# Optimization experiments

Hardware: AMD Instinct MI355X
Metric: run time of the kernel (lower is better)

The kernel has to match this reference:

```python
import jax, jax.numpy as jnp
import numpy as np

B, N, DIM, H, DH = 2, 2048, 1024, 16, 64
ALPHA = 32.0 ** 2  # stable_softmax alpha
SCALE = DH ** -0.5


def rotate_half(x):
    # interleaved pairs: (x0, x1, x2, x3, ...) -> (-x1, x0, -x3, x2, ...)
    xp = x.reshape(x.shape[:-1] + (-1, 2))
    return jnp.stack((-xp[..., 1], xp[..., 0]), axis=-1).reshape(x.shape)


def apply_rotary(freqs, t):
    # freqs: [n, d]; t: [b, h, n, d]
    return t * jnp.cos(freqs) + rotate_half(t) * jnp.sin(freqs)


def setup_inputs() -> dict:
    key = jax.random.key(0)
    k0, k1, k2, k3 = jax.random.split(key, 4)
    x = jax.random.normal(k0, (B, N, DIM), jnp.float32)
    rotary_pos_emb = jax.random.normal(k1, (N, DH), jnp.float32)
    w_qkv = jax.random.normal(k2, (DIM, 3 * H * DH), jnp.float32) / np.sqrt(DIM)
    w_out = jax.random.normal(k3, (H * DH, DIM), jnp.float32) / np.sqrt(H * DH)
    b_out = jnp.zeros((DIM,), jnp.float32)
    return {"x": x, "rotary_pos_emb": rotary_pos_emb, "w_qkv": w_qkv,
            "w_out": w_out, "b_out": b_out}


def reference(x, rotary_pos_emb, w_qkv, w_out, b_out):
    b, n, _ = x.shape
    qkv = x @ w_qkv                                  # [b, n, 3*h*d]
    q, k, v = jnp.split(qkv, 3, axis=-1)
    to_heads = lambda t: t.reshape(b, n, H, DH).transpose(0, 2, 1, 3)  # [b,h,n,d]
    q, k, v = map(to_heads, (q, k, v))
    freqs = rotary_pos_emb[:n]
    # source applies rotary emb to q, k AND v
    q = apply_rotary(freqs, q)
    k = apply_rotary(freqs, k)
    v = apply_rotary(freqs, v)
    q = q * SCALE
    dots = jnp.einsum('bhid,bhjd->bhij', q, k)       # [b,h,n,n]
    mask_value = -jnp.finfo(dots.dtype).max
    causal = jnp.triu(jnp.ones((n, n), bool), 1)
    dots = jnp.where(causal, mask_value, dots)
    # stable softmax: divide by alpha, subtract detached max, rescale
    t = dots / ALPHA
    t = t - jax.lax.stop_gradient(jnp.max(t, axis=-1, keepdims=True))
    attn = jax.nn.softmax(t * ALPHA, axis=-1)
    out = jnp.einsum('bhij,bhjd->bhid', attn, v)     # [b,h,n,d]
    out = out.transpose(0, 2, 1, 3).reshape(b, n, H * DH)
    return out @ w_out + b_out
```

## Files before the change

kernel.cpp:

```cpp
#include <hip/hip_runtime.h>
#include <stdint.h>

#define DEV __device__ __forceinline__

typedef __bf16 bf16x8 __attribute__((ext_vector_type(8)));
typedef float  f32x4  __attribute__((ext_vector_type(4)));
typedef short  s16x8  __attribute__((ext_vector_type(8)));

constexpr int Bb   = 2;
constexpr int Nn   = 2048;
constexpr int DIMc = 1024;
constexpr int Hh   = 16;
constexpr int DHc  = 64;
constexpr int BN   = Bb * Nn;
constexpr int QKVC = 3 * Hh * DHc;

DEV ushort f2b(float f) {
  uint32_t u = __float_as_uint(f);
  u += 0x7fffu + ((u >> 16) & 1u);
  return (ushort)(u >> 16);
}

DEV void gload16(const void* g, void* l) {
  __builtin_amdgcn_global_load_lds(
      (const __attribute__((address_space(1))) void*)(uintptr_t)g,
      (__attribute__((address_space(3))) void*)(uint32_t)(uintptr_t)l,
      16, 0, 0);
}

DEV f32x4 mfma16(bf16x8 a, bf16x8 b, f32x4 c) {
  return __builtin_amdgcn_mfma_f32_16x16x32_bf16(a, b, c, 0, 0, 0);
}

DEV uint32_t cvtpk(float lo, float hi) {
  uint32_t r;
  asm("v_cvt_pk_bf16_f32 %0, %1, %2" : "=v"(r) : "v"(lo), "v"(hi));
  return r;
}


__global__ void k_cast_x(const float* __restrict__ x, ushort* __restrict__ xb) {
  int i = blockIdx.x * 256 + threadIdx.x;
  size_t base = (size_t)i * 8;
  s16x8 v;
#pragma unroll
  for (int j = 0; j < 8; ++j) v[j] = (short)f2b(x[base + j]);
  *(s16x8*)(xb + base) = v;
}

__global__ void k_sincos(const float* __restrict__ rope, float2* __restrict__ csT) {
  int i = blockIdx.x * 256 + threadIdx.x;
  float t = rope[i];
  float s, c;
  sincosf(t, &s, &c);
  csT[i] = make_float2(c, s);
}

__global__ void k_transpose_cast(const float* __restrict__ src, ushort* __restrict__ dst,
                                 int K, int Ncols) {
  __shared__ float tile[32][33];
  int nb = blockIdx.x * 32, kb = blockIdx.y * 32;
  int tx = threadIdx.x, ty = threadIdx.y;
#pragma unroll
  for (int i = 0; i < 4; ++i) {
    int k = ty + i * 8;
    tile[k][tx] = src[(size_t)(kb + k) * Ncols + nb + tx];
  }
  __syncthreads();
#pragma unroll
  for (int i = 0; i < 4; ++i) {
    int n = ty + i * 8;
    dst[(size_t)(nb + n) * K + kb + tx] = f2b(tile[tx][n]);
  }
}

DEV void gemm_core(const ushort* __restrict__ A, const ushort* __restrict__ Bt,
                   int rowBase, int colBase, ushort* lA, ushort* lB,
                   f32x4 (&acc)[4][4]) {
  const int tid = threadIdx.x;
  const int lane = tid & 63, w = tid >> 6;
  const int wm = w >> 1, wn = w & 1;
  const int g = lane >> 4, l16 = lane & 15;
  const f32x4 zero = {0.f, 0.f, 0.f, 0.f};
#pragma unroll
  for (int i = 0; i < 4; ++i)
#pragma unroll
    for (int j = 0; j < 4; ++j) acc[i][j] = zero;

  const int c0row = tid >> 2,          c0kc = (tid & 3) ^ ((c0row >> 1) & 3);
  const int c1row = (256 + tid) >> 2,  c1kc = (tid & 3) ^ ((c1row >> 1) & 3);
  const ushort* gA0 = A  + (size_t)(rowBase + c0row) * DIMc + c0kc * 8;
  const ushort* gA1 = A  + (size_t)(rowBase + c1row) * DIMc + c1kc * 8;
  const ushort* gB0 = Bt + (size_t)(colBase + c0row) * DIMc + c0kc * 8;
  const ushort* gB1 = Bt + (size_t)(colBase + c1row) * DIMc + c1kc * 8;
  ushort* lDst0 = (ushort*)((size_t)(0 * 256 + w * 64) * 8 * 2);
  const size_t o0 = (size_t)(0 * 256 + w * 64) * 8;
  const size_t o1 = (size_t)(1 * 256 + w * 64) * 8;

  gload16(gA0, lA + o0);
  gload16(gB0, lB + o0);
  gload16(gA1, lA + o1);
  gload16(gB1, lB + o1);

  for (int k0 = 0; k0 < DIMc; k0 += 32) {
    const int cur = (k0 >> 5) & 1;
    ushort* cA = lA + cur * (128 * 32);
    ushort* cB = lB + cur * (128 * 32);
    if (k0 + 32 < DIMc) {
      ushort* nA = lA + (cur ^ 1) * (128 * 32);
      ushort* nB = lB + (cur ^ 1) * (128 * 32);
      int kn = k0 + 32;
      gload16(gA0 + kn, nA + o0);
      gload16(gB0 + kn, nB + o0);
      gload16(gA1 + kn, nA + o1);
      gload16(gB1 + kn, nB + o1);
      asm volatile("s_waitcnt vmcnt(4)" ::: "memory");
    } else {
      asm volatile("s_waitcnt vmcnt(0)" ::: "memory");
    }
    __builtin_amdgcn_s_barrier();

    bf16x8 af[4], bfr[4];
#pragma unroll
    for (int f = 0; f < 4; ++f) {
      int r  = wm * 64 + f * 16 + l16;
      int r2 = wn * 64 + f * 16 + l16;
      af[f]  = *(const bf16x8*)&cA[r * 32 + ((g ^ ((r >> 1) & 3)) << 3)];
      bfr[f] = *(const bf16x8*)&cB[r2 * 32 + ((g ^ ((r2 >> 1) & 3)) << 3)];
    }
#pragma unroll
    for (int i = 0; i < 4; ++i)
#pragma unroll
      for (int j = 0; j < 4; ++j)
        acc[i][j] = mfma16(af[i], bfr[j], acc[i][j]);

    __builtin_amdgcn_s_barrier();
  }
}

__global__ __launch_bounds__(256) void k_gemm_qkv(
    const ushort* __restrict__ xb, const ushort* __restrict__ wT,
    const float2* __restrict__ csT,
    ushort* __restrict__ Qd, ushort* __restrict__ Kd, ushort* __restrict__ Vd) {
  __shared__ ushort lA[2 * 128 * 32];
  __shared__ ushort lB[2 * 128 * 32];
  f32x4 acc[4][4];
  const int rowBase = blockIdx.y * 128, colBase = blockIdx.x * 128;
  gemm_core(xb, wT, rowBase, colBase, lA, lB, acc);

  const int lane = threadIdx.x & 63, w = threadIdx.x >> 6;
  const int wm = w >> 1, wn = w & 1;
  const int g = lane >> 4, l16 = lane & 15;
#pragma unroll
  for (int fm = 0; fm < 4; ++fm) {
#pragma unroll
    for (int fn = 0; fn < 4; ++fn) {
      int col = colBase + wn * 64 + fn * 16 + l16;
      int sel = col >> 10, hc = col & 1023;
      int h = hc >> 6, d = hc & 63;
      float sgn = (d & 1) ? 1.f : -1.f;
#pragma unroll
      for (int r = 0; r < 4; ++r) {
        float t  = acc[fm][fn][r];
        float tp = __shfl_xor(t, 1);
        int row = rowBase + wm * 64 + fm * 16 + 4 * g + r;
        int b = row >> 11, n = row & 2047;
        float2 cs = csT[n * 64 + d];
        float rv = t * cs.x + sgn * tp * cs.y;
        if (sel == 0) {
          Qd[((size_t)(b * Hh + h) * Nn + n) * DHc + d] = f2b(rv * 0.125f);
        } else if (sel == 1) {
          Kd[((size_t)(b * Hh + h) * Nn + n) * DHc + d] = f2b(rv);
        } else {
          Vd[((size_t)(b * Hh + h) * DHc + d) * Nn + n] = f2b(rv);
        }
      }
    }
  }
}


DEV void stageKV(const ushort* __restrict__ Kh, const ushort* __restrict__ Vh,
                 ushort* lKb, ushort* lVb, int kt, int tid, int w) {
#pragma unroll
  for (int s = 0; s < 2; ++s) {
    int c = s * 256 + tid;
    int row = c >> 3, jst = c & 7;
    int jl = jst ^ (row & 7);
    gload16(Kh + (size_t)(kt * 64 + row) * DHc + jl * 8,
            lKb + (size_t)(s * 256 + w * 64) * 8);
    gload16(Vh + (size_t)row * Nn + kt * 64 + jl * 8,
            lVb + (size_t)(s * 256 + w * 64) * 8);
  }
}

DEV void attn_step(const ushort* lKc, const ushort* lVc, char* lPw,
                   const bf16x8 (&q)[2], f32x4 (&o)[4], float& m, float& l,
                   int kBase, int qg, bool diag, int g, int l16) {
  const f32x4 zero = {0.f, 0.f, 0.f, 0.f};
  f32x4 s[4];
#pragma unroll
  for (int jt = 0; jt < 4; ++jt) s[jt] = zero;

#pragma unroll
  for (int jt = 0; jt < 4; ++jt) {
    int jr = jt * 16 + l16;
#pragma unroll
    for (int d0 = 0; d0 < 2; ++d0) {
      bf16x8 kb = *(const bf16x8*)&lKc[jr * 64 + (((d0 * 4 + g) ^ (jr & 7)) << 3)];
      s[jt] = mfma16(kb, q[d0], s[jt]);
    }
  }

  if (diag) {
#pragma unroll
    for (int jt = 0; jt < 4; ++jt)
#pragma unroll
      for (int r = 0; r < 4; ++r) {
        int j = kBase + jt * 16 + 4 * g + r;
        if (j > qg) s[jt][r] = -3.0e38f;
      }
  }

  float tmax = fmaxf(fmaxf(fmaxf(s[0][0], s[0][1]), fmaxf(s[0][2], s[0][3])),
                     fmaxf(fmaxf(s[1][0], s[1][1]), fmaxf(s[1][2], s[1][3])));
  tmax = fmaxf(tmax, fmaxf(fmaxf(fmaxf(s[2][0], s[2][1]), fmaxf(s[2][2], s[2][3])),
                           fmaxf(fmaxf(s[3][0], s[3][1]), fmaxf(s[3][2], s[3][3]))));
  tmax = fmaxf(tmax, __shfl_xor(tmax, 16));
  tmax = fmaxf(tmax, __shfl_xor(tmax, 32));

  if (!__all(tmax <= m + 8.f)) {
    float mnew = fmaxf(m, tmax);
    float sc = __expf(m - mnew);
#pragma unroll
    for (int dt = 0; dt < 4; ++dt) o[dt] *= sc;
    l *= sc;
    m = mnew;
  }

  float ps = 0.f;
#pragma unroll
  for (int jt = 0; jt < 4; ++jt)
#pragma unroll
    for (int r = 0; r < 4; ++r) {
      float p = __expf(s[jt][r] - m);
      s[jt][r] = p;
      ps += p;
    }
  ps += __shfl_xor(ps, 16);
  ps += __shfl_xor(ps, 32);
  l += ps;

  const int sw = (l16 & 7) << 4;
  char* prow = lPw + l16 * 128;
#pragma unroll
  for (int jt = 0; jt < 4; ++jt) {
    int jo = (jt * 16 + 4 * g) * 2;
    *(uint32_t*)(prow + (jo ^ sw))       = cvtpk(s[jt][0], s[jt][1]);
    *(uint32_t*)(prow + ((jo + 4) ^ sw)) = cvtpk(s[jt][2], s[jt][3]);
  }

  bf16x8 pa[2];
#pragma unroll
  for (int jh = 0; jh < 2; ++jh)
    pa[jh] = *(const bf16x8*)(prow + (((jh * 32 + 8 * g) * 2) ^ sw));
#pragma unroll
  for (int dt = 0; dt < 4; ++dt) {
    int d = dt * 16 + l16;
#pragma unroll
    for (int jh = 0; jh < 2; ++jh) {
      bf16x8 vb = *(const bf16x8*)&lVc[d * 64 + (((jh * 4 + g) ^ (d & 7)) << 3)];
      o[dt] = mfma16(vb, pa[jh], o[dt]);
    }
  }
}

DEV void attn_epi(ushort* __restrict__ ao, int bh, int n, int g,
                  f32x4 (&o)[4], float l) {
  const int b = bh >> 4, h = bh & 15;
  float inv = 1.f / l;
  ushort* dst = ao + (size_t)(b * Nn + n) * (Hh * DHc) + h * 64;
#pragma unroll
  for (int dt = 0; dt < 4; ++dt) {
    uint2 pkd;
    pkd.x = cvtpk(o[dt][0] * inv, o[dt][1] * inv);
    pkd.y = cvtpk(o[dt][2] * inv, o[dt][3] * inv);
    *(uint2*)(dst + dt * 16 + 4 * g) = pkd;
  }
}

__global__ __launch_bounds__(256) void k_attn(
    const ushort* __restrict__ Qd, const ushort* __restrict__ Kd,
    const ushort* __restrict__ Vd, ushort* __restrict__ ao) {
  __shared__ ushort lK[2][64 * 64];
  __shared__ ushort lV[2][64 * 64];
  __shared__ char   lP[4][16 * 128];
  const int tid = threadIdx.x;
  const int lane = tid & 63, w = tid >> 6;
  const int g = lane >> 4, l16 = lane & 15;
  const int bh = blockIdx.y;
  const int p = blockIdx.x;
  const int tA = p, tB = 31 - p;
  const int last = tB;
  const ushort* Qh = Qd + (size_t)bh * Nn * DHc;
  const ushort* Kh = Kd + (size_t)bh * Nn * DHc;
  const ushort* Vh = Vd + (size_t)bh * DHc * Nn;

  const int qgA = tA * 64 + w * 16 + l16;
  const int qgB = tB * 64 + w * 16 + l16;

  bf16x8 qA[2], qB[2];
#pragma unroll
  for (int d0 = 0; d0 < 2; ++d0) {
    qA[d0] = *(const bf16x8*)(Qh + (size_t)qgA * DHc + d0 * 32 + g * 8);
    qB[d0] = *(const bf16x8*)(Qh + (size_t)qgB * DHc + d0 * 32 + g * 8);
  }

  const f32x4 zero = {0.f, 0.f, 0.f, 0.f};
  f32x4 oA[4], oB[4];
#pragma unroll
  for (int dt = 0; dt < 4; ++dt) { oA[dt] = zero; oB[dt] = zero; }
  float mA = -3.0e38f, lA_ = 0.f, mB = -3.0e38f, lB_ = 0.f;

  stageKV(Kh, Vh, lK[0], lV[0], 0, tid, w);

  for (int kt = 0; kt <= last; ++kt) {
    const int cur = kt & 1;
    if (kt < last) {
      stageKV(Kh, Vh, lK[cur ^ 1], lV[cur ^ 1], kt + 1, tid, w);
      asm volatile("s_waitcnt vmcnt(4)" ::: "memory");
    } else {
      asm volatile("s_waitcnt vmcnt(0)" ::: "memory");
    }
    __builtin_amdgcn_s_barrier();

    attn_step(lK[cur], lV[cur], lP[w], qB, oB, mB, lB_, kt * 64, qgB, kt == tB, g, l16);
    if (kt <= tA)
      attn_step(lK[cur], lV[cur], lP[w], qA, oA, mA, lA_, kt * 64, qgA, kt == tA, g, l16);

    __builtin_amdgcn_s_barrier();
  }

  attn_epi(ao, bh, qgA, g, oA, lA_);
  attn_epi(ao, bh, qgB, g, oB, lB_);
}

__global__ __launch_bounds__(256) void k_gemm_out(
    const ushort* __restrict__ ao, const ushort* __restrict__ wT,
    const float* __restrict__ bias, float* __restrict__ out) {
  __shared__ ushort lA[2 * 128 * 32];
  __shared__ ushort lB[2 * 128 * 32];
  f32x4 acc[4][4];
  const int rowBase = blockIdx.y * 128, colBase = blockIdx.x * 128;
  gemm_core(ao, wT, rowBase, colBase, lA, lB, acc);

  const int lane = threadIdx.x & 63, w = threadIdx.x >> 6;
  const int wm = w >> 1, wn = w & 1;
  const int g = lane >> 4, l16 = lane & 15;
#pragma unroll
  for (int fm = 0; fm < 4; ++fm)
#pragma unroll
    for (int fn = 0; fn < 4; ++fn) {
      int col = colBase + wn * 64 + fn * 16 + l16;
#pragma unroll
      for (int r = 0; r < 4; ++r) {
        int row = rowBase + wm * 64 + fm * 16 + 4 * g + r;
        out[(size_t)row * DIMc + col] = acc[fm][fn][r] + bias[col];
      }
    }
}

extern "C" void kernel_launch(void* const* d_in, const int* in_sizes, int n_in,
                              void* d_out, int out_size, void* d_ws, size_t ws_size,
                              hipStream_t stream) {
  const float* x     = (const float*)d_in[0];
  const float* rope  = (const float*)d_in[1];
  const float* w_qkv = (const float*)d_in[2];
  const float* w_out = (const float*)d_in[3];
  const float* b_out = (const float*)d_in[4];
  float* out = (float*)d_out;

  char* ws = (char*)d_ws;
  ushort* xb    = (ushort*)(ws);
  ushort* wqkvT = (ushort*)(ws + 8388608);
  ushort* woutT = (ushort*)(ws + 14680064);
  float2* csT   = (float2*)(ws + 16777216);
  ushort* Qd    = (ushort*)(ws + 17825792);
  ushort* Kd    = (ushort*)(ws + 26214400);
  ushort* Vd    = (ushort*)(ws + 34603008);
  ushort* ao    = (ushort*)(ws + 42991616);

  hipLaunchKernelGGL(k_cast_x, dim3(2048), dim3(256), 0, stream, x, xb);
  hipLaunchKernelGGL(k_transpose_cast, dim3(QKVC / 32, DIMc / 32), dim3(32, 8), 0, stream,
                     w_qkv, wqkvT, DIMc, QKVC);
  hipLaunchKernelGGL(k_transpose_cast, dim3(DIMc / 32, DIMc / 32), dim3(32, 8), 0, stream,
                     w_out, woutT, DIMc, DIMc);
  hipLaunchKernelGGL(k_sincos, dim3(Nn * DHc / 256), dim3(256), 0, stream, rope, csT);
  hipLaunchKernelGGL(k_gemm_qkv, dim3(QKVC / 128, BN / 128), dim3(256), 0, stream,
                     xb, wqkvT, csT, Qd, Kd, Vd);
  hipLaunchKernelGGL(k_attn, dim3(16, Bb * Hh), dim3(256), 0, stream, Qd, Kd, Vd, ao);
  hipLaunchKernelGGL(k_gemm_out, dim3(DIMc / 128, BN / 128), dim3(256), 0, stream,
                     ao, woutT, b_out, out);
}
```

Before: 135.6 us.

## Rewrite QKV GEMM with 256x256 tiles, 8 waves, and interleaved load/MFMA schedule

Replaces the QKV projection GEMM, which used 128x128 tiles and 4 waves, with a 256x256-tile kernel of 8 waves that stages 64-wide K slices. Global-to-LDS loads for the next tile are interleaved between four MFMA quadrants, with explicit barriers, waitcnt and setprio to overlap memory with compute. This aims to raise data reuse and hide load latency. The grid shrinks to 12x16=192 blocks, which may underfill the 256 CUs and raises register pressure.

After: 150.3 us. 1.11x slower.

```diff
diff --git a/kernel.cpp b/kernel.cpp
--- a/kernel.cpp
+++ b/kernel.cpp
@@ -71,6 +71,169 @@
   for (int i = 0; i < 4; ++i) {
     int n = ty + i * 8;
     dst[(size_t)(nb + n) * K + kb + tx] = f2b(tile[tx][n]);
+  }
+}
+
+__global__ __launch_bounds__(512, 2) void k_gemm_qkv(
+    const ushort* __restrict__ xb, const ushort* __restrict__ wT,
+    const float2* __restrict__ csT,
+    ushort* __restrict__ Qd, ushort* __restrict__ Kd, ushort* __restrict__ Vd) {
+  __shared__ ushort lA[2 * 256 * 64];
+  __shared__ ushort lB[2 * 256 * 64];
+  const int tid = threadIdx.x;
+  const int lane = tid & 63, wid = tid >> 6;
+  const int wm = wid >> 2, wn = wid & 3;
+  const int g = lane >> 4, l16 = lane & 15, l7 = lane & 7;
+  const int rowBase = blockIdx.y * 256, colBase = blockIdx.x * 256;
+  constexpr int NT = DIMc / 64;
+
+  const int sr0 = tid >> 3;
+  const int gc  = (tid & 7) ^ (sr0 & 7);
+  const ushort* gA = xb + (size_t)(rowBase + sr0) * DIMc + gc * 8;
+  const ushort* gB = wT + (size_t)(colBase + sr0) * DIMc + gc * 8;
+
+#define STAGE_A(T, H) do { \
+    gload16(gA + (size_t)((H) * 128) * DIMc + (T) * 64, lA + (((T) & 1) * 16384 + (H) * 8192 + wid * 512)); \
+    gload16(gA + (size_t)((H) * 128 + 64) * DIMc + (T) * 64, lA + (((T) & 1) * 16384 + (H) * 8192 + 4096 + wid * 512)); \
+  } while (0)
+#define STAGE_B(T, H) do { \
+    gload16(gB + (size_t)((H) * 128) * DIMc + (T) * 64, lB + (((T) & 1) * 16384 + (H) * 8192 + wid * 512)); \
+    gload16(gB + (size_t)((H) * 128 + 64) * DIMc + (T) * 64, lB + (((T) & 1) * 16384 + (H) * 8192 + 4096 + wid * 512)); \
+  } while (0)
+
+  f32x4 acc[8][4];
+  const f32x4 zero = {0.f, 0.f, 0.f, 0.f};
+#pragma unroll
+  for (int i = 0; i < 8; ++i)
+#pragma unroll
+    for (int j = 0; j < 4; ++j) acc[i][j] = zero;
+
+  bf16x8 aF[4][2], bF[4][2];
+
+  STAGE_A(0, 0); STAGE_A(0, 1); STAGE_B(0, 0); STAGE_B(0, 1);
+  STAGE_B(1, 0); STAGE_B(1, 1);
+  asm volatile("s_waitcnt vmcnt(4)" ::: "memory");
+  __builtin_amdgcn_s_barrier();
+
+  for (int kt = 0; kt < NT; ++kt) {
+    const ushort* cA = lA + (kt & 1) * 16384;
+    const ushort* cB = lB + (kt & 1) * 16384;
+
+#pragma unroll
+    for (int mf = 0; mf < 4; ++mf)
+#pragma unroll
+      for (int ks = 0; ks < 2; ++ks)
+        aF[mf][ks] = *(const bf16x8*)&cA[(wm * 128 + mf * 16 + l16) * 64 + (((ks * 4 + g) ^ l7) << 3)];
+#pragma unroll
+    for (int nf = 0; nf < 2; ++nf)
+#pragma unroll
+      for (int ks = 0; ks < 2; ++ks)
+        bF[nf][ks] = *(const bf16x8*)&cB[(wn * 64 + nf * 16 + l16) * 64 + (((ks * 4 + g) ^ l7) << 3)];
+    if (kt + 1 < NT) STAGE_A(kt + 1, 0);
+    __builtin_amdgcn_s_barrier();
+    asm volatile("s_waitcnt lgkmcnt(0)" ::: "memory");
+    __builtin_amdgcn_sched_barrier(0);
+    __builtin_amdgcn_s_setprio(1);
+#pragma unroll
+    for (int mf = 0; mf < 4; ++mf)
+#pragma unroll
+      for (int nf = 0; nf < 2; ++nf)
+#pragma unroll
+        for (int ks = 0; ks < 2; ++ks)
+          acc[mf][nf] = mfma16(aF[mf][ks], bF[nf][ks], acc[mf][nf]);
+    __builtin_amdgcn_s_setprio(0);
+    __builtin_amdgcn_sched_barrier(0);
+    __builtin_amdgcn_s_barrier();
+
+#pragma unroll
+    for (int nf = 0; nf < 2; ++nf)
+#pragma unroll
+      for (int ks = 0; ks < 2; ++ks)
+        bF[2 + nf][ks] = *(const bf16x8*)&cB[(wn * 64 + (2 + nf) * 16 + l16) * 64 + (((ks * 4 + g) ^ l7) << 3)];
+    if (kt + 1 < NT) STAGE_A(kt + 1, 1);
+    __builtin_amdgcn_s_barrier();
+    asm volatile("s_waitcnt lgkmcnt(0)" ::: "memory");
+    __builtin_amdgcn_sched_barrier(0);
+    __builtin_amdgcn_s_setprio(1);
+#pragma unroll
+    for (int mf = 0; mf < 4; ++mf)
+#pragma unroll
+      for (int nf = 0; nf < 2; ++nf)
+#pragma unroll
+        for (int ks = 0; ks < 2; ++ks)
+          acc[mf][2 + nf] = mfma16(aF[mf][ks], bF[2 + nf][ks], acc[mf][2 + nf]);
+    __builtin_amdgcn_s_setprio(0);
+    __builtin_amdgcn_sched_barrier(0);
+    __builtin_amdgcn_s_barrier();
+
+#pragma unroll
+    for (int mf = 0; mf < 4; ++mf)
+#pragma unroll
+      for (int ks = 0; ks < 2; ++ks)
+        aF[mf][ks] = *(const bf16x8*)&cA[(wm * 128 + 64 + mf * 16 + l16) * 64 + (((ks * 4 + g) ^ l7) << 3)];
+    if (kt + 2 < NT) STAGE_B(kt + 2, 0);
+    __builtin_amdgcn_s_barrier();
+    asm volatile("s_waitcnt lgkmcnt(0)" ::: "memory");
+    __builtin_amdgcn_sched_barrier(0);
+    __builtin_amdgcn_s_setprio(1);
+#pragma unroll
+    for (int mf = 0; mf < 4; ++mf)
+#pragma unroll
+      for (int nf = 0; nf < 2; ++nf)
+#pragma unroll
+        for (int ks = 0; ks < 2; ++ks)
+          acc[4 + mf][nf] = mfma16(aF[mf][ks], bF[nf][ks], acc[4 + mf][nf]);
+    __builtin_amdgcn_s_setprio(0);
+    __builtin_amdgcn_sched_barrier(0);
+    __builtin_amdgcn_s_barrier();
+
+    if (kt + 2 < NT) {
+      STAGE_B(kt + 2, 1);
+      asm volatile("s_waitcnt vmcnt(4)" ::: "memory");
+    } else {
+      asm volatile("s_waitcnt vmcnt(0)" ::: "memory");
+    }
+    __builtin_amdgcn_s_barrier();
+    __builtin_amdgcn_s_setprio(1);
+#pragma unroll
+    for (int mf = 0; mf < 4; ++mf)
+#pragma unroll
+      for (int nf = 0; nf < 2; ++nf)
+#pragma unroll
+        for (int ks = 0; ks < 2; ++ks)
+          acc[4 + mf][2 + nf] = mfma16(aF[mf][ks], bF[2 + nf][ks], acc[4 + mf][2 + nf]);
+    __builtin_amdgcn_s_setprio(0);
+    __builtin_amdgcn_sched_barrier(0);
+    __builtin_amdgcn_s_barrier();
+  }
+#undef STAGE_A
+#undef STAGE_B
+
+#pragma unroll
+  for (int mf = 0; mf < 8; ++mf) {
+#pragma unroll
+    for (int nf = 0; nf < 4; ++nf) {
+      int col = colBase + wn * 64 + nf * 16 + l16;
+      int sel = col >> 10, hc = col & 1023;
+      int h = hc >> 6, d = hc & 63;
+      float sgn = (d & 1) ? 1.f : -1.f;
+#pragma unroll
+      for (int r = 0; r < 4; ++r) {
+        float t  = acc[mf][nf][r];
+        float tp = __shfl_xor(t, 1);
+        int row = rowBase + wm * 128 + mf * 16 + 4 * g + r;
+        int b = row >> 11, n = row & 2047;
+        float2 cs = csT[n * 64 + d];
+        float rv = t * cs.x + sgn * tp * cs.y;
+        if (sel == 0) {
+          Qd[((size_t)(b * Hh + h) * Nn + n) * DHc + d] = f2b(rv * 0.125f);
+        } else if (sel == 1) {
+          Kd[((size_t)(b * Hh + h) * Nn + n) * DHc + d] = f2b(rv);
+        } else {
+          Vd[((size_t)(b * Hh + h) * DHc + d) * Nn + n] = f2b(rv);
+        }
+      }
+    }
   }
 }
 
@@ -93,7 +256,6 @@
   const ushort* gA1 = A  + (size_t)(rowBase + c1row) * DIMc + c1kc * 8;
   const ushort* gB0 = Bt + (size_t)(colBase + c0row) * DIMc + c0kc * 8;
   const ushort* gB1 = Bt + (size_t)(colBase + c1row) * DIMc + c1kc * 8;
-  ushort* lDst0 = (ushort*)((size_t)(0 * 256 + w * 64) * 8 * 2);
   const size_t o0 = (size_t)(0 * 256 + w * 64) * 8;
   const size_t o1 = (size_t)(1 * 256 + w * 64) * 8;
 
@@ -135,47 +297,6 @@
         acc[i][j] = mfma16(af[i], bfr[j], acc[i][j]);
 
     __builtin_amdgcn_s_barrier();
-  }
-}
-
-__global__ __launch_bounds__(256) void k_gemm_qkv(
-    const ushort* __restrict__ xb, const ushort* __restrict__ wT,
-    const float2* __restrict__ csT,
-    ushort* __restrict__ Qd, ushort* __restrict__ Kd, ushort* __restrict__ Vd) {
-  __shared__ ushort lA[2 * 128 * 32];
-  __shared__ ushort lB[2 * 128 * 32];
-  f32x4 acc[4][4];
-  const int rowBase = blockIdx.y * 128, colBase = blockIdx.x * 128;
-  gemm_core(xb, wT, rowBase, colBase, lA, lB, acc);
-
-  const int lane = threadIdx.x & 63, w = threadIdx.x >> 6;
-  const int wm = w >> 1, wn = w & 1;
-  const int g = lane >> 4, l16 = lane & 15;
-#pragma unroll
-  for (int fm = 0; fm < 4; ++fm) {
-#pragma unroll
-    for (int fn = 0; fn < 4; ++fn) {
-      int col = colBase + wn * 64 + fn * 16 + l16;
-      int sel = col >> 10, hc = col & 1023;
-      int h = hc >> 6, d = hc & 63;
-      float sgn = (d & 1) ? 1.f : -1.f;
-#pragma unroll
-      for (int r = 0; r < 4; ++r) {
-        float t  = acc[fm][fn][r];
-        float tp = __shfl_xor(t, 1);
-        int row = rowBase + wm * 64 + fm * 16 + 4 * g + r;
-        int b = row >> 11, n = row & 2047;
-        float2 cs = csT[n * 64 + d];
-        float rv = t * cs.x + sgn * tp * cs.y;
-        if (sel == 0) {
-          Qd[((size_t)(b * Hh + h) * Nn + n) * DHc + d] = f2b(rv * 0.125f);
-        } else if (sel == 1) {
-          Kd[((size_t)(b * Hh + h) * Nn + n) * DHc + d] = f2b(rv);
-        } else {
-          Vd[((size_t)(b * Hh + h) * DHc + d) * Nn + n] = f2b(rv);
-        }
-      }
-    }
   }
 }
 
@@ -396,7 +517,7 @@
   hipLaunchKernelGGL(k_transpose_cast, dim3(DIMc / 32, DIMc / 32), dim3(32, 8), 0, stream,
                      w_out, woutT, DIMc, DIMc);
   hipLaunchKernelGGL(k_sincos, dim3(Nn * DHc / 256), dim3(256), 0, stream, rope, csT);
-  hipLaunchKernelGGL(k_gemm_qkv, dim3(QKVC / 128, BN / 128), dim3(256), 0, stream,
+  hipLaunchKernelGGL(k_gemm_qkv, dim3(QKVC / 256, BN / 256), dim3(512), 0, stream,
                      xb, wqkvT, csT, Qd, Kd, Vd);
   hipLaunchKernelGGL(k_attn, dim3(16, Bb * Hh), dim3(256), 0, stream, Qd, Kd, Vd, ao);
   hipLaunchKernelGGL(k_gemm_out, dim3(DIMc / 128, BN / 128), dim3(256), 0, stream,
```

## Triple-buffer GEMM LDS tiles with one barrier per k-step

Applied to the files above, without the earlier changes.

Changes the shared GEMM core from a double-buffered to a three-stage LDS pipeline. Loads are issued two k-steps ahead, and each iteration now has a single barrier instead of two. The aim is to hide global-to-LDS latency behind the MFMA work and cut synchronisation in the QKV and output projection GEMMs. The cost is 50% more LDS per block, which may lower occupancy.

New measurement: 131.1 us. 1.03x faster.

```diff
diff --git a/kernel.cpp b/kernel.cpp
--- a/kernel.cpp
+++ b/kernel.cpp
@@ -93,48 +93,54 @@
   const ushort* gA1 = A  + (size_t)(rowBase + c1row) * DIMc + c1kc * 8;
   const ushort* gB0 = Bt + (size_t)(colBase + c0row) * DIMc + c0kc * 8;
   const ushort* gB1 = Bt + (size_t)(colBase + c1row) * DIMc + c1kc * 8;
-  ushort* lDst0 = (ushort*)((size_t)(0 * 256 + w * 64) * 8 * 2);
   const size_t o0 = (size_t)(0 * 256 + w * 64) * 8;
   const size_t o1 = (size_t)(1 * 256 + w * 64) * 8;
-
-  gload16(gA0, lA + o0);
-  gload16(gB0, lB + o0);
-  gload16(gA1, lA + o1);
-  gload16(gB1, lB + o1);
-
+  constexpr int BUF = 128 * 32;
+
+  gload16(gA0,      lA + o0);        gload16(gB0,      lB + o0);
+  gload16(gA1,      lA + o1);        gload16(gB1,      lB + o1);
+  gload16(gA0 + 32, lA + BUF + o0);  gload16(gB0 + 32, lB + BUF + o0);
+  gload16(gA1 + 32, lA + BUF + o1);  gload16(gB1 + 32, lB + BUF + o1);
+  asm volatile("s_waitcnt vmcnt(4)" ::: "memory");
+  __builtin_amdgcn_s_barrier();
+
+  int cur = 0;
   for (int k0 = 0; k0 < DIMc; k0 += 32) {
-    const int cur = (k0 >> 5) & 1;
-    ushort* cA = lA + cur * (128 * 32);
-    ushort* cB = lB + cur * (128 * 32);
-    if (k0 + 32 < DIMc) {
-      ushort* nA = lA + (cur ^ 1) * (128 * 32);
-      ushort* nB = lB + (cur ^ 1) * (128 * 32);
-      int kn = k0 + 32;
-      gload16(gA0 + kn, nA + o0);
-      gload16(gB0 + kn, nB + o0);
-      gload16(gA1 + kn, nA + o1);
-      gload16(gB1 + kn, nB + o1);
-      asm volatile("s_waitcnt vmcnt(4)" ::: "memory");
-    } else {
-      asm volatile("s_waitcnt vmcnt(0)" ::: "memory");
-    }
-    __builtin_amdgcn_s_barrier();
+    const ushort* cA = lA + cur * BUF;
+    const ushort* cB = lB + cur * BUF;
 
     bf16x8 af[4], bfr[4];
 #pragma unroll
     for (int f = 0; f < 4; ++f) {
       int r  = wm * 64 + f * 16 + l16;
       int r2 = wn * 64 + f * 16 + l16;
-      af[f]  = *(const bf16x8*)&cA[r * 32 + ((g ^ ((r >> 1) & 3)) << 3)];
+      af[f]  = *(const bf16x8*)&cA[r  * 32 + ((g ^ ((r  >> 1) & 3)) << 3)];
       bfr[f] = *(const bf16x8*)&cB[r2 * 32 + ((g ^ ((r2 >> 1) & 3)) << 3)];
     }
+
+    const int kn = k0 + 64;
+    if (kn < DIMc) {
+      int st = cur + 2; if (st >= 3) st -= 3;
+      ushort* nA = lA + st * BUF;
+      ushort* nB = lB + st * BUF;
+      gload16(gA0 + kn, nA + o0);  gload16(gB0 + kn, nB + o0);
+      gload16(gA1 + kn, nA + o1);  gload16(gB1 + kn, nB + o1);
+    }
+
 #pragma unroll
     for (int i = 0; i < 4; ++i)
 #pragma unroll
       for (int j = 0; j < 4; ++j)
         acc[i][j] = mfma16(af[i], bfr[j], acc[i][j]);
 
+    if (kn < DIMc) {
+      asm volatile("s_waitcnt vmcnt(4)" ::: "memory");
+    } else if (k0 + 32 < DIMc) {
+      asm volatile("s_waitcnt vmcnt(0)" ::: "memory");
+    }
+    asm volatile("s_waitcnt lgkmcnt(0)" ::: "memory");
     __builtin_amdgcn_s_barrier();
+    cur += 1; if (cur == 3) cur = 0;
   }
 }
 
@@ -142,8 +148,8 @@
     const ushort* __restrict__ xb, const ushort* __restrict__ wT,
     const float2* __restrict__ csT,
     ushort* __restrict__ Qd, ushort* __restrict__ Kd, ushort* __restrict__ Vd) {
-  __shared__ ushort lA[2 * 128 * 32];
-  __shared__ ushort lB[2 * 128 * 32];
+  __shared__ ushort lA[3 * 128 * 32];
+  __shared__ ushort lB[3 * 128 * 32];
   f32x4 acc[4][4];
   const int rowBase = blockIdx.y * 128, colBase = blockIdx.x * 128;
   gemm_core(xb, wT, rowBase, colBase, lA, lB, acc);
@@ -348,8 +354,8 @@
 __global__ __launch_bounds__(256) void k_gemm_out(
     const ushort* __restrict__ ao, const ushort* __restrict__ wT,
     const float* __restrict__ bias, float* __restrict__ out) {
-  __shared__ ushort lA[2 * 128 * 32];
-  __shared__ ushort lB[2 * 128 * 32];
+  __shared__ ushort lA[3 * 128 * 32];
+  __shared__ ushort lB[3 * 128 * 32];
   f32x4 acc[4][4];
   const int rowBase = blockIdx.y * 128, colBase = blockIdx.x * 128;
   gemm_core(ao, wT, rowBase, colBase, lA, lB, acc);
```
